# Kernel optimization log

Hardware: AMD Instinct MI355X
Metric: run time of the kernel (lower is better)

## Reference

```python
import jax, jax.numpy as jnp
import numpy as np

B, C, HIMG, WIMG = 32, 3, 224, 224
P, D, L, F, H, NC = 16, 768, 12, 3072, 12, 1000
S = (HIMG // P) * (WIMG // P)  # 196 tokens
DH = D // H                    # 64 per head


def setup_inputs() -> dict:
    key = jax.random.key(0)
    ks = jax.random.split(key, 12)
    rn = lambda i, shape, sc: jax.random.normal(ks[i], shape, jnp.float32) * sc
    return dict(
        x=rn(0, (B, C, HIMG, WIMG), 1.0),
        conv_w=rn(1, (D, C, P, P), 0.02),
        conv_b=jnp.zeros((D,), jnp.float32),
        pos_embed=rn(2, (S, D), 0.02),
        ln1_s=jnp.ones((L, D), jnp.float32),
        ln1_b=jnp.zeros((L, D), jnp.float32),
        wq=rn(3, (L, D, D), 0.02),
        wk=rn(4, (L, D, D), 0.02),
        wv=rn(5, (L, D, D), 0.02),
        ln2_s=jnp.ones((L, D), jnp.float32),
        ln2_b=jnp.zeros((L, D), jnp.float32),
        w1=rn(6, (L, D, F), 0.02),
        b1=jnp.zeros((L, F), jnp.float32),
        w2=rn(7, (L, F, D), 0.02),
        b2=jnp.zeros((L, D), jnp.float32),
        fc_w=rn(8, (D, NC), 0.02),
        fc_b=jnp.zeros((NC,), jnp.float32),
    )


def _layernorm(x, scale, bias, eps=1e-5):
    m = x.mean(-1, keepdims=True)
    v = ((x - m) ** 2).mean(-1, keepdims=True)
    return (x - m) * jax.lax.rsqrt(v + eps) * scale + bias


def reference(x, conv_w, conv_b, pos_embed, ln1_s, ln1_b, wq, wk, wv,
              ln2_s, ln2_b, w1, b1, w2, b2, fc_w, fc_b):
    # patch embedding: stride-P conv, then b c h w -> b (h w) c, add pos embed
    h = jax.lax.conv_general_dilated(
        x, conv_w, (P, P), 'VALID',
        dimension_numbers=('NCHW', 'OIHW', 'NCHW'))
    h = h + conv_b[None, :, None, None]
    h = h.reshape(B, D, S).transpose(0, 2, 1) + pos_embed  # [B,S,D]

    # NOTE: original scales attention logits by 1/sqrt(seq_len), not 1/sqrt(d_head)
    scale = 1.0 / jnp.sqrt(jnp.float32(S))

    def layer(hx, p):
        l1s, l1b, Wq, Wk, Wv, l2s, l2b, W1, B1, W2, B2 = p
        xn = _layernorm(hx, l1s, l1b)
        q = (xn @ Wq).reshape(B, S, H, DH)
        k = (xn @ Wk).reshape(B, S, H, DH)
        v = (xn @ Wv).reshape(B, S, H, DH)
        att = jax.nn.softmax(jnp.einsum('bshd,bthd->bhst', q, k) * scale, axis=-1)
        o = jnp.einsum('bhst,bthd->bshd', att, v).reshape(B, S, D)
        hx = hx + o
        y = _layernorm(hx, l2s, l2b) @ W1 + B1
        y = jax.nn.gelu(y, approximate=False) @ W2 + B2
        return hx + y, None

    h, _ = jax.lax.scan(layer, h, (ln1_s, ln1_b, wq, wk, wv,
                                   ln2_s, ln2_b, w1, b1, w2, b2))
    return h.mean(axis=1) @ fc_w + fc_b  # [B, num_classes]
```

## Files before the change

kernel.cpp:

```cpp
#include <hip/hip_runtime.h>
#include <hip/hip_bf16.h>

typedef __attribute__((ext_vector_type(8))) short bf16x8;
typedef __attribute__((ext_vector_type(4))) short bf16x4;
typedef __attribute__((ext_vector_type(4))) float f32x4;

#define DEVI static __device__ __forceinline__

DEVI unsigned short f2bf(float f) {
  __hip_bfloat16 h = __float2bfloat16(f);
  return __builtin_bit_cast(unsigned short, h);
}

DEVI f32x4 mfma16(bf16x8 a, bf16x8 b, f32x4 c) {
  return __builtin_amdgcn_mfma_f32_16x16x32_bf16(a, b, c, 0, 0, 0);
}

DEVI void gload16(const unsigned short* g, unsigned short* l) {
  __builtin_amdgcn_global_load_lds(
      (const __attribute__((address_space(1))) void*)g,
      (__attribute__((address_space(3))) void*)l, 16, 0, 0);
}

DEVI float erf_fast(float x) {
  float ax = fabsf(x);
  float t = 1.f / (1.f + 0.3275911f * ax);
  float poly = ((((1.061405429f * t - 1.453152027f) * t + 1.421413741f) * t -
                 0.284496736f) * t + 0.254829592f) * t;
  float e = __expf(-x * x);
  float er = 1.f - poly * e;
  return copysignf(er, x);
}

__global__ __launch_bounds__(256) void k_im2col(const float* __restrict__ x,
                                                unsigned short* __restrict__ A) {
  int t = blockIdx.x * 256 + threadIdx.x;
  int m = t / 192;
  int qq = t - m * 192;
  int kk = qq * 4;
  int c = kk >> 8;
  int r = kk & 255;
  int i = r >> 4;
  int j = r & 15;
  int b = m / 196;
  int s = m - b * 196;
  int ph = s / 14;
  int pw = s - ph * 14;
  const float* src = x + ((size_t)((b * 3 + c) * 224 + ph * 16 + i)) * 224 + pw * 16 + j;
  f32x4 v = *reinterpret_cast<const f32x4*>(src);
  bf16x4 o;
  o[0] = (short)f2bf(v[0]); o[1] = (short)f2bf(v[1]);
  o[2] = (short)f2bf(v[2]); o[3] = (short)f2bf(v[3]);
  *reinterpret_cast<bf16x4*>(A + (size_t)m * 768 + kk) = o;
}

__global__ __launch_bounds__(256) void k_cvt(const float* __restrict__ in,
                                             unsigned short* __restrict__ out) {
  int t = blockIdx.x * 256 + threadIdx.x;
  f32x4 v = *reinterpret_cast<const f32x4*>(in + (size_t)t * 4);
  bf16x4 o;
  o[0] = (short)f2bf(v[0]); o[1] = (short)f2bf(v[1]);
  o[2] = (short)f2bf(v[2]); o[3] = (short)f2bf(v[3]);
  *reinterpret_cast<bf16x4*>(out + (size_t)t * 4) = o;
}

DEVI void transpose_tile(const float* __restrict__ in, unsigned short* __restrict__ out,
                         int K, int N, int kt, int nt, unsigned short (*tile)[68]) {
  int r = threadIdx.x >> 4;
  int c4 = (threadIdx.x & 15) * 4;
  int k0 = kt * 64, n0 = nt * 64;
#pragma unroll
  for (int rr0 = 0; rr0 < 4; rr0++) {
    int rr = r + rr0 * 16;
    f32x4 v = *reinterpret_cast<const f32x4*>(in + (size_t)(k0 + rr) * N + n0 + c4);
    bf16x4 o;
    o[0] = (short)f2bf(v[0]); o[1] = (short)f2bf(v[1]);
    o[2] = (short)f2bf(v[2]); o[3] = (short)f2bf(v[3]);
    *reinterpret_cast<bf16x4*>(&tile[rr][c4]) = o;
  }
  __syncthreads();
#pragma unroll
  for (int rr0 = 0; rr0 < 4; rr0++) {
    int rr = r + rr0 * 16;
    bf16x4 o;
    o[0] = (short)tile[c4 + 0][rr];
    o[1] = (short)tile[c4 + 1][rr];
    o[2] = (short)tile[c4 + 2][rr];
    o[3] = (short)tile[c4 + 3][rr];
    *reinterpret_cast<bf16x4*>(out + (size_t)(n0 + rr) * K + k0 + c4) = o;
  }
}

__global__ __launch_bounds__(256) void k_wconvert(
    const float* __restrict__ wq, const float* __restrict__ wk, const float* __restrict__ wv,
    const float* __restrict__ w1, const float* __restrict__ w2,
    unsigned short* __restrict__ wqkvT, unsigned short* __restrict__ w1T,
    unsigned short* __restrict__ w2T) {
  __shared__ unsigned short tile[64][68];
  int bid = blockIdx.x;
  if (bid < 432) {
    int mm = bid / 144, t2 = bid - mm * 144;
    const float* in = (mm == 0) ? wq : ((mm == 1) ? wk : wv);
    transpose_tile(in, wqkvT + (size_t)mm * 768 * 768, 768, 768, t2 / 12, t2 % 12, tile);
  } else if (bid < 1008) {
    int t2 = bid - 432;
    transpose_tile(w1, w1T, 768, 3072, t2 / 48, t2 % 48, tile);
  } else {
    int t2 = bid - 1008;
    transpose_tile(w2, w2T, 3072, 768, t2 / 12, t2 % 12, tile);
  }
}

template <int RED>
__global__ __launch_bounds__(256) void k_ln(float* __restrict__ h,
                                            const float* __restrict__ part,
                                            const float* __restrict__ sc,
                                            const float* __restrict__ bi,
                                            unsigned short* __restrict__ xn) {
  int wave = threadIdx.x >> 6, lane = threadIdx.x & 63;
  int row = blockIdx.x * 4 + wave;
  float* hr = h + (size_t)row * 768;
  const float* pr = part + (size_t)row * 768;
  f32x4 v[3];
  float sum = 0.f;
#pragma unroll
  for (int i = 0; i < 3; i++) {
    v[i] = *reinterpret_cast<const f32x4*>(hr + i * 256 + lane * 4);
    if (RED) {
      f32x4 pv = *reinterpret_cast<const f32x4*>(pr + i * 256 + lane * 4);
#pragma unroll
      for (int c = 0; c < 4; c++) v[i][c] += pv[c];
      *reinterpret_cast<f32x4*>(hr + i * 256 + lane * 4) = v[i];
    }
    sum += v[i][0] + v[i][1] + v[i][2] + v[i][3];
  }
#pragma unroll
  for (int m = 1; m < 64; m <<= 1) sum += __shfl_xor(sum, m, 64);
  float mean = sum * (1.f / 768.f);
  float var = 0.f;
#pragma unroll
  for (int i = 0; i < 3; i++)
#pragma unroll
    for (int c = 0; c < 4; c++) { float d = v[i][c] - mean; var += d * d; }
#pragma unroll
  for (int m = 1; m < 64; m <<= 1) var += __shfl_xor(var, m, 64);
  float rs = rsqrtf(var * (1.f / 768.f) + 1e-5f);
#pragma unroll
  for (int i = 0; i < 3; i++) {
    int col = i * 256 + lane * 4;
    f32x4 s4 = *reinterpret_cast<const f32x4*>(sc + col);
    f32x4 b4 = *reinterpret_cast<const f32x4*>(bi + col);
    bf16x4 o;
#pragma unroll
    for (int c = 0; c < 4; c++) o[c] = (short)f2bf((v[i][c] - mean) * rs * s4[c] + b4[c]);
    *reinterpret_cast<bf16x4*>(xn + (size_t)row * 768 + col) = o;
  }
}

template <int EPI>
__global__ __launch_bounds__(256) void k_gemm(
    const unsigned short* __restrict__ A, const unsigned short* __restrict__ Bt, int K,
    int nks, const float* __restrict__ bias, const float* __restrict__ aux,
    float* __restrict__ outF, float* __restrict__ pOut) {
  __shared__ __align__(16) unsigned short As[2][128 * 32];
  __shared__ __align__(16) unsigned short Bs[2][128 * 32];

  int GX = gridDim.x, GY = gridDim.y, GZ = gridDim.z;
  int nb = GX * GY * GZ;
  int lin = (blockIdx.z * GY + blockIdx.y) * GX + blockIdx.x;
  int q = nb >> 3, r8 = nb & 7;
  int xcd = lin & 7, off = lin >> 3;
  int wid = (xcd < r8 ? xcd * (q + 1) : r8 * (q + 1) + (xcd - r8) * q) + off;
  int t2 = GX * GY;
  int sz = wid / t2;
  int w2 = wid - sz * t2;
  const int GM = 8;
  int per = GM * GX;
  int g = w2 / per;
  int first_m = g * GM;
  int gm = min(GM, GY - first_m);
  int rem = w2 - g * per;
  int mt = first_m + rem % gm;
  int nt = rem / gm;
  int m0 = mt * 128, n0 = nt * 128;
  int kb = sz * nks * 32;

  int tid = threadIdx.x;
  int wave = tid >> 6, lane = tid & 63;
  int wm = (wave >> 1) * 64, wn = (wave & 1) * 64;
  int lr = lane & 15, lg = lane >> 4;

  f32x4 acc[4][4];
  const f32x4 fz = {0.f, 0.f, 0.f, 0.f};
#pragma unroll
  for (int i = 0; i < 4; i++)
#pragma unroll
    for (int j = 0; j < 4; j++) acc[i][j] = fz;

  int srow = wave * 16 + (lane >> 2);
  int scol = (lane & 3) * 8;
  const unsigned short* Ag = A + (size_t)(m0 + srow) * K + scol + kb;
  const unsigned short* Bg = Bt + (size_t)(n0 + srow) * K + scol + kb;
  int lofs = wave * 16 * 32;

#pragma unroll
  for (int j = 0; j < 2; j++) {
    gload16(Ag + (size_t)j * 64 * K, &As[0][lofs + j * 64 * 32]);
    gload16(Bg + (size_t)j * 64 * K, &Bs[0][lofs + j * 64 * 32]);
  }
  __syncthreads();

  for (int kt = 0; kt < nks - 1; kt++) {
    int cur = kt & 1;
    int k0 = (kt + 1) << 5;
#pragma unroll
    for (int j = 0; j < 2; j++) {
      gload16(Ag + (size_t)j * 64 * K + k0, &As[cur ^ 1][lofs + j * 64 * 32]);
      gload16(Bg + (size_t)j * 64 * K + k0, &Bs[cur ^ 1][lofs + j * 64 * 32]);
    }
    bf16x8 a[4], b[4];
#pragma unroll
    for (int i = 0; i < 4; i++) {
      a[i] = *reinterpret_cast<const bf16x8*>(&As[cur][(wm + i * 16 + lr) * 32 + lg * 8]);
      b[i] = *reinterpret_cast<const bf16x8*>(&Bs[cur][(wn + i * 16 + lr) * 32 + lg * 8]);
    }
#pragma unroll
    for (int mi = 0; mi < 4; mi++)
#pragma unroll
      for (int ni = 0; ni < 4; ni++) acc[mi][ni] = mfma16(a[mi], b[ni], acc[mi][ni]);
    __syncthreads();
  }
  {
    int cur = (nks - 1) & 1;
    bf16x8 a[4], b[4];
#pragma unroll
    for (int i = 0; i < 4; i++) {
      a[i] = *reinterpret_cast<const bf16x8*>(&As[cur][(wm + i * 16 + lr) * 32 + lg * 8]);
      b[i] = *reinterpret_cast<const bf16x8*>(&Bs[cur][(wn + i * 16 + lr) * 32 + lg * 8]);
    }
#pragma unroll
    for (int mi = 0; mi < 4; mi++)
#pragma unroll
      for (int ni = 0; ni < 4; ni++) acc[mi][ni] = mfma16(a[mi], b[ni], acc[mi][ni]);
  }

#pragma unroll
  for (int mi = 0; mi < 4; mi++) {
    int mb = m0 + wm + mi * 16 + lg * 4;
    int bb = mb / 196;
    int s0 = mb - bb * 196;
#pragma unroll
    for (int ni = 0; ni < 4; ni++) {
      int n = n0 + wn + ni * 16 + lr;
      int s = s0;
#pragma unroll
      for (int r = 0; r < 4; r++) {
        int m = mb + r;
        float val = acc[mi][ni][r];
        if (EPI == 0) {
          outF[(size_t)m * 768 + n] = val + bias[n] + aux[(size_t)s * 768 + n];
          s++;
          if (s == 196) s = 0;
        } else {
          if (sz == 0) outF[(size_t)m * 768 + n] += val + bias[n];
          else pOut[(size_t)m * 768 + n] = val;
        }
      }
    }
  }
}

__global__ __launch_bounds__(256) void k_mean_r(const float* __restrict__ h,
                                                const float* __restrict__ part,
                                                float* __restrict__ hm) {
  int b = blockIdx.x, d = blockIdx.y * 256 + threadIdx.x;
  float acc = 0.f;
  for (int s = 0; s < 196; s++) {
    size_t i = (size_t)(b * 196 + s) * 768 + d;
    acc += h[i] + part[i];
  }
  hm[b * 768 + d] = acc * (1.f / 196.f);
}

template <int EPI>
__global__ __launch_bounds__(512, 2) void k_gemm256p(
    const unsigned short* __restrict__ A, const unsigned short* __restrict__ Bt,
    const float* __restrict__ bias, unsigned short* __restrict__ outB) {
  const int K = 768, NK = 24;
  __shared__ __align__(16) unsigned short LDS[4][16384];
  const int MVALID = 6272;

  int GX = gridDim.x, GY = gridDim.y;
  int nb = GX * GY;
  int lin = blockIdx.y * GX + blockIdx.x;
  int q = nb >> 3, r8 = nb & 7;
  int xcd = lin & 7, off = lin >> 3;
  int wid = (xcd < r8 ? xcd * (q + 1) : r8 * (q + 1) + (xcd - r8) * q) + off;
  const int GM = 4;
  int per = GM * GX;
  int g = wid / per;
  int first_m = g * GM;
  int gm = min(GM, GY - first_m);
  int rem = wid - g * per;
  int mt = first_m + rem % gm;
  int nt = rem / gm;
  int m0 = mt * 256, n0 = nt * 256;

  int tid = threadIdx.x;
  int w = tid >> 6, lane = tid & 63;
  int wm = w >> 2, wn = w & 3;
  int lr = lane & 15, lg = lane >> 4;

  f32x4 acc[8][4];
  const f32x4 fz = {0.f, 0.f, 0.f, 0.f};
#pragma unroll
  for (int i = 0; i < 8; i++)
#pragma unroll
    for (int j = 0; j < 4; j++) acc[i][j] = fz;

  int srow = w * 16 + (lane >> 2);
  int scol = ((lane & 3) ^ ((lane >> 3) & 3)) * 8;
  const unsigned short* Ag = A + (size_t)(m0 + srow) * K + scol;
  const unsigned short* Bg = Bt + (size_t)(n0 + srow) * K + scol;
  int ldst = w * 512;

  int colsw = (lg ^ ((lr >> 1) & 3)) * 8;
  int rofA = wm * 4096 + lr * 32 + colsw;
  int rofB = 8192 + wn * 2048 + lr * 32 + colsw;

#define STAGEA(kt)                                                          \
  {                                                                         \
    unsigned short* d_ = &LDS[(kt) & 3][0];                                 \
    const unsigned short* a_ = Ag + (kt) * 32;                              \
    gload16(a_, d_ + ldst);                                                 \
    gload16(a_ + (size_t)128 * K, d_ + 4096 + ldst);                        \
  }
#define STAGEB(kt)                                                          \
  {                                                                         \
    unsigned short* d_ = &LDS[(kt) & 3][0];                                 \
    const unsigned short* b_ = Bg + (kt) * 32;                              \
    gload16(b_, d_ + 8192 + ldst);                                          \
    gload16(b_ + (size_t)128 * K, d_ + 12288 + ldst);                       \
  }

#define KTILE(ktv, VMSTR, STG, LAST)                                         \
  {                                                                          \
    const int kt_ = (ktv);                                                   \
    const unsigned short* buf_ = &LDS[kt_ & 3][0];                           \
    bf16x8 afr[8], bfr[2];                                                   \
    _Pragma("unroll") for (int mi = 0; mi < 8; mi++) afr[mi] =               \
        *reinterpret_cast<const bf16x8*>(buf_ + rofA + mi * 512);            \
    _Pragma("unroll") for (int ni = 0; ni < 2; ni++) bfr[ni] =               \
        *reinterpret_cast<const bf16x8*>(buf_ + rofB + ni * 512);            \
    if (STG) STAGEA(kt_ + 3);                                                \
    asm volatile("s_waitcnt lgkmcnt(0)" ::: "memory");                       \
    __builtin_amdgcn_sched_barrier(0);                                       \
    __builtin_amdgcn_s_setprio(1);                                           \
    _Pragma("unroll") for (int mi = 0; mi < 8; mi++)                         \
        _Pragma("unroll") for (int ni = 0; ni < 2; ni++)                     \
            acc[mi][ni] = mfma16(afr[mi], bfr[ni], acc[mi][ni]);             \
    __builtin_amdgcn_s_setprio(0);                                           \
    __builtin_amdgcn_s_barrier();                                            \
    _Pragma("unroll") for (int ni = 0; ni < 2; ni++) bfr[ni] =               \
        *reinterpret_cast<const bf16x8*>(buf_ + rofB + (2 + ni) * 512);      \
    if (STG) STAGEB(kt_ + 3);                                                \
    asm volatile("s_waitcnt lgkmcnt(0)" ::: "memory");                       \
    __builtin_amdgcn_sched_barrier(0);                                       \
    __builtin_amdgcn_s_setprio(1);                                           \
    _Pragma("unroll") for (int mi = 0; mi < 8; mi++)                         \
        _Pragma("unroll") for (int ni = 0; ni < 2; ni++)                     \
            acc[mi][2 + ni] = mfma16(afr[mi], bfr[ni], acc[mi][2 + ni]);     \
    __builtin_amdgcn_s_setprio(0);                                           \
    if (!LAST) {                                                             \
      asm volatile("s_waitcnt vmcnt(" VMSTR ")" ::: "memory");               \
      __builtin_amdgcn_s_barrier();                                          \
    }                                                                        \
  }

  STAGEA(0); STAGEB(0);
  STAGEA(1); STAGEB(1);
  STAGEA(2); STAGEB(2);
  asm volatile("s_waitcnt vmcnt(8)" ::: "memory");
  __builtin_amdgcn_s_barrier();

  for (int kt = 0; kt < NK - 3; kt++) KTILE(kt, "8", true, false);
  KTILE(NK - 3, "4", false, false);
  KTILE(NK - 2, "0", false, false);
  KTILE(NK - 1, "0", false, true);
#undef KTILE
#undef STAGEA
#undef STAGEB

  if (EPI == 1) {
#pragma unroll
    for (int ni = 0; ni < 4; ni++) {
      int n = n0 + wn * 64 + ni * 16 + lr;
      int which = (n >= 1536) ? 2 : ((n >= 768) ? 1 : 0);
      int n7 = n - which * 768;
      int hd = n7 >> 6, dh = n7 & 63;
      unsigned short* ob = outB + (size_t)which * 4816896 + dh;
#pragma unroll
      for (int mi = 0; mi < 8; mi++) {
        int mb = m0 + wm * 128 + mi * 16 + lg * 4;
        if (mb >= MVALID) continue;
        int bb = mb / 196;
        int s = mb - bb * 196;
#pragma unroll
        for (int r = 0; r < 4; r++) {
          ob[((size_t)((bb * 12 + hd) * 196 + s) << 6)] = f2bf(acc[mi][ni][r]);
          s++;
          if (s == 196) { s = 0; bb++; }
        }
      }
    }
  } else {
#pragma unroll
    for (int mi = 0; mi < 8; mi++) {
      int mb = m0 + wm * 128 + mi * 16 + lg * 4;
      if (mb >= MVALID) continue;
#pragma unroll
      for (int ni = 0; ni < 4; ni++) {
        int n = n0 + wn * 64 + ni * 16 + lr;
#pragma unroll
        for (int r = 0; r < 4; r++) {
          int m = mb + r;
          float u = acc[mi][ni][r] + bias[n];
          float gg = 0.5f * u * (1.f + erf_fast(u * 0.70710678118654752f));
          outB[(size_t)m * 3072 + n] = f2bf(gg);
        }
      }
    }
  }
}

__global__ __launch_bounds__(512) void k_attn(const unsigned short* __restrict__ q,
                                              const unsigned short* __restrict__ k,
                                              const unsigned short* __restrict__ v,
                                              float* __restrict__ h) {
  __shared__ __align__(16) unsigned short Kl[208][72];
  __shared__ __align__(16) unsigned short Vt[64][248];
  __shared__ __align__(16) unsigned short Sc[8][16][232];
  int bh = blockIdx.x;
  int b = bh / 12, hh = bh - b * 12;
  size_t base = (size_t)bh * 196 * 64;
  int tid = threadIdx.x, wave = tid >> 6, lane = tid & 63;
  int lr = lane & 15, lg = lane >> 4;

  const bf16x8 bz = {0, 0, 0, 0, 0, 0, 0, 0};
  for (int u = tid; u < 208 * 8; u += 512) {
    int row = u >> 3, c8 = (u & 7) * 8;
    bf16x8 val = bz;
    if (row < 196) val = *reinterpret_cast<const bf16x8*>(k + base + row * 64 + c8);
    *reinterpret_cast<bf16x8*>(&Kl[row][c8]) = val;
  }
  for (int u = tid; u < 224 * 8; u += 512) {
    int t = u >> 3, d8 = (u & 7) * 8;
    bf16x8 val = bz;
    if (t < 196) val = *reinterpret_cast<const bf16x8*>(v + base + t * 64 + d8);
#pragma unroll
    for (int i = 0; i < 8; i++) Vt[d8 + i][t] = (unsigned short)val[i];
  }
  for (int i2 = lane; i2 < 256; i2 += 64) Sc[wave][i2 >> 4][208 + (i2 & 15)] = 0;
  __syncthreads();

  const float scale = 1.f / 14.f;
  for (int st = wave; st < 13; st += 8) {
    int qb = st * 16;
    int s = qb + lr;
    bf16x8 aq0 = bz, aq1 = bz;
    if (s < 196) {
      aq0 = *reinterpret_cast<const bf16x8*>(q + base + (size_t)s * 64 + lg * 8);
      aq1 = *reinterpret_cast<const bf16x8*>(q + base + (size_t)s * 64 + 32 + lg * 8);
    }
    f32x4 sc[13];
#pragma unroll
    for (int t = 0; t < 13; t++) {
      bf16x8 bk0 = *reinterpret_cast<const bf16x8*>(&Kl[t * 16 + lr][lg * 8]);
      bf16x8 bk1 = *reinterpret_cast<const bf16x8*>(&Kl[t * 16 + lr][32 + lg * 8]);
      f32x4 z = {0.f, 0.f, 0.f, 0.f};
      z = mfma16(aq0, bk0, z);
      z = mfma16(aq1, bk1, z);
      sc[t] = z;
    }
    float mx[4] = {-1e30f, -1e30f, -1e30f, -1e30f};
#pragma unroll
    for (int t = 0; t < 13; t++) {
      int tc = t * 16 + lr;
#pragma unroll
      for (int r = 0; r < 4; r++) {
        float xv = (tc < 196) ? sc[t][r] * scale : -1e30f;
        sc[t][r] = xv;
        mx[r] = fmaxf(mx[r], xv);
      }
    }
#pragma unroll
    for (int r = 0; r < 4; r++)
#pragma unroll
      for (int mm = 1; mm < 16; mm <<= 1) mx[r] = fmaxf(mx[r], __shfl_xor(mx[r], mm, 64));
    float sm[4] = {0.f, 0.f, 0.f, 0.f};
#pragma unroll
    for (int t = 0; t < 13; t++)
#pragma unroll
      for (int r = 0; r < 4; r++) {
        float e = __expf(sc[t][r] - mx[r]);
        sc[t][r] = e;
        sm[r] += e;
      }
#pragma unroll
    for (int r = 0; r < 4; r++)
#pragma unroll
      for (int mm = 1; mm < 16; mm <<= 1) sm[r] += __shfl_xor(sm[r], mm, 64);
    float inv[4];
#pragma unroll
    for (int r = 0; r < 4; r++) inv[r] = 1.f / sm[r];
#pragma unroll
    for (int t = 0; t < 13; t++)
#pragma unroll
      for (int r = 0; r < 4; r++)
        Sc[wave][lg * 4 + r][t * 16 + lr] = f2bf(sc[t][r] * inv[r]);
    asm volatile("s_waitcnt lgkmcnt(0)" ::: "memory");
    bf16x8 ap[7];
#pragma unroll
    for (int ks = 0; ks < 7; ks++)
      ap[ks] = *reinterpret_cast<const bf16x8*>(&Sc[wave][lr][ks * 32 + lg * 8]);
#pragma unroll
    for (int nt = 0; nt < 4; nt++) {
      f32x4 o = {0.f, 0.f, 0.f, 0.f};
#pragma unroll
      for (int ks = 0; ks < 7; ks++) {
        bf16x8 bv = *reinterpret_cast<const bf16x8*>(&Vt[nt * 16 + lr][ks * 32 + lg * 8]);
        o = mfma16(ap[ks], bv, o);
      }
#pragma unroll
      for (int r = 0; r < 4; r++) {
        int s2 = qb + lg * 4 + r;
        if (s2 < 196) h[(size_t)(b * 196 + s2) * 768 + hh * 64 + nt * 16 + lr] += o[r];
      }
    }
  }
}

__global__ __launch_bounds__(256) void k_fc(const float* __restrict__ hm,
                                            const float* __restrict__ w,
                                            const float* __restrict__ bias,
                                            float* __restrict__ out) {
  int b = blockIdx.x, n = blockIdx.y * 256 + threadIdx.x;
  if (n >= 1000) return;
  float acc = bias[n];
  for (int d = 0; d < 768; d++) acc += hm[b * 768 + d] * w[d * 1000 + n];
  out[b * 1000 + n] = acc;
}

extern "C" void kernel_launch(void* const* d_in, const int* in_sizes, int n_in,
                              void* d_out, int out_size, void* d_ws, size_t ws_size,
                              hipStream_t stream) {
  const float* x      = (const float*)d_in[0];
  const float* conv_w = (const float*)d_in[1];
  const float* conv_b = (const float*)d_in[2];
  const float* pos    = (const float*)d_in[3];
  const float* ln1_s  = (const float*)d_in[4];
  const float* ln1_b  = (const float*)d_in[5];
  const float* wq     = (const float*)d_in[6];
  const float* wk     = (const float*)d_in[7];
  const float* wv     = (const float*)d_in[8];
  const float* ln2_s  = (const float*)d_in[9];
  const float* ln2_b  = (const float*)d_in[10];
  const float* w1     = (const float*)d_in[11];
  const float* b1     = (const float*)d_in[12];
  const float* w2     = (const float*)d_in[13];
  const float* b2     = (const float*)d_in[14];
  const float* fc_w   = (const float*)d_in[15];
  const float* fc_b   = (const float*)d_in[16];
  float* out = (float*)d_out;

  char* p = (char*)d_ws;
  auto alloc = [&](size_t bytes) {
    char* r = p;
    p += (bytes + 255) & ~(size_t)255;
    return r;
  };
  const size_t M = 6272, MP = 6400, QSZ = 4816896;
  float* h              = (float*)alloc(M * 768 * 4);
  unsigned short* xn    = (unsigned short*)alloc(MP * 768 * 2);
  unsigned short* qkv   = (unsigned short*)alloc(3 * QSZ * 2);
  unsigned short* y1    = (unsigned short*)alloc(MP * 3072 * 2);
  unsigned short* wqkvT = (unsigned short*)alloc((size_t)2304 * 768 * 2);
  unsigned short* w1T   = (unsigned short*)alloc((size_t)3072 * 768 * 2);
  unsigned short* w2T   = (unsigned short*)alloc((size_t)3072 * 768 * 2);
  float* hm             = (float*)alloc(32 * 768 * 4);
  unsigned short* cwB   = qkv;
  float* part           = (float*)qkv;

  k_cvt<<<576, 256, 0, stream>>>(conv_w, cwB);
  k_im2col<<<4704, 256, 0, stream>>>(x, xn);
  k_gemm<0><<<dim3(6, 49, 1), 256, 0, stream>>>(xn, cwB, 768, 24, conv_b, pos, h, nullptr);

  for (int l = 0; l < 12; l++) {
    k_wconvert<<<1584, 256, 0, stream>>>(
        wq + (size_t)l * 589824, wk + (size_t)l * 589824, wv + (size_t)l * 589824,
        w1 + (size_t)l * 2359296, w2 + (size_t)l * 2359296, wqkvT, w1T, w2T);
    if (l == 0)
      k_ln<0><<<1568, 256, 0, stream>>>(h, nullptr, ln1_s, ln1_b, xn);
    else
      k_ln<1><<<1568, 256, 0, stream>>>(h, part, ln1_s + l * 768, ln1_b + l * 768, xn);
    k_gemm256p<1><<<dim3(9, 25), 512, 0, stream>>>(xn, wqkvT, nullptr, qkv);
    k_attn<<<384, 512, 0, stream>>>(qkv, qkv + QSZ, qkv + 2 * QSZ, h);
    k_ln<0><<<1568, 256, 0, stream>>>(h, nullptr, ln2_s + l * 768, ln2_b + l * 768, xn);
    k_gemm256p<2><<<dim3(12, 25), 512, 0, stream>>>(xn, w1T, b1 + (size_t)l * 3072, y1);
    k_gemm<3><<<dim3(6, 49, 2), 256, 0, stream>>>(y1, w2T, 3072, 48, b2 + (size_t)l * 768,
                                                  nullptr, h, part);
  }
  k_mean_r<<<dim3(32, 3), 256, 0, stream>>>(h, part, hm);
  k_fc<<<dim3(32, 4), 256, 0, stream>>>(hm, fc_w, fc_b, out);
}
```

Before: 2.923 ms.

## Hoist all-layer weight conversion into one launch and narrow W2 GEMM tile

When workspace allows, all 12 layers' weights are transposed and converted to bf16 in a single large kernel before the layer loop, replacing 12 per-layer conversion launches that sat on the critical path between layers. The k_gemm kernel is templated on the N tile width, and the FFN down-projection now uses 128x64 tiles with twice as many blocks to improve occupancy and load balance. This costs more workspace memory and reduces per-block reuse in the W2 GEMM.

```diff
diff --git a/kernel.cpp b/kernel.cpp
--- a/kernel.cpp
+++ b/kernel.cpp
@@ -91,13 +91,11 @@
   }
 }
 
-__global__ __launch_bounds__(256) void k_wconvert(
-    const float* __restrict__ wq, const float* __restrict__ wk, const float* __restrict__ wv,
-    const float* __restrict__ w1, const float* __restrict__ w2,
-    unsigned short* __restrict__ wqkvT, unsigned short* __restrict__ w1T,
-    unsigned short* __restrict__ w2T) {
-  __shared__ unsigned short tile[64][68];
-  int bid = blockIdx.x;
+DEVI void wconvert_body(const float* wq, const float* wk, const float* wv,
+                        const float* w1, const float* w2,
+                        unsigned short* wqkvT, unsigned short* w1T,
+                        unsigned short* w2T, int bid,
+                        unsigned short (*tile)[68]) {
   if (bid < 432) {
     int mm = bid / 144, t2 = bid - mm * 144;
     const float* in = (mm == 0) ? wq : ((mm == 1) ? wk : wv);
@@ -109,6 +107,28 @@
     int t2 = bid - 1008;
     transpose_tile(w2, w2T, 3072, 768, t2 / 12, t2 % 12, tile);
   }
+}
+
+__global__ __launch_bounds__(256) void k_wconvert(
+    const float* __restrict__ wq, const float* __restrict__ wk, const float* __restrict__ wv,
+    const float* __restrict__ w1, const float* __restrict__ w2,
+    unsigned short* __restrict__ wqkvT, unsigned short* __restrict__ w1T,
+    unsigned short* __restrict__ w2T) {
+  __shared__ unsigned short tile[64][68];
+  wconvert_body(wq, wk, wv, w1, w2, wqkvT, w1T, w2T, blockIdx.x, tile);
+}
+
+__global__ __launch_bounds__(256) void k_wconvert_all(
+    const float* __restrict__ wq, const float* __restrict__ wk, const float* __restrict__ wv,
+    const float* __restrict__ w1, const float* __restrict__ w2,
+    unsigned short* __restrict__ wqkvT, unsigned short* __restrict__ w1T,
+    unsigned short* __restrict__ w2T) {
+  __shared__ unsigned short tile[64][68];
+  int l = blockIdx.x / 1584, bid = blockIdx.x - l * 1584;
+  wconvert_body(wq + (size_t)l * 589824, wk + (size_t)l * 589824, wv + (size_t)l * 589824,
+                w1 + (size_t)l * 2359296, w2 + (size_t)l * 2359296,
+                wqkvT + (size_t)l * 1769472, w1T + (size_t)l * 2359296,
+                w2T + (size_t)l * 2359296, bid, tile);
 }
 
 template <int RED>
@@ -157,13 +177,15 @@
   }
 }
 
-template <int EPI>
+template <int EPI, int BN>
 __global__ __launch_bounds__(256) void k_gemm(
     const unsigned short* __restrict__ A, const unsigned short* __restrict__ Bt, int K,
     int nks, const float* __restrict__ bias, const float* __restrict__ aux,
     float* __restrict__ outF, float* __restrict__ pOut) {
+  constexpr int NI = BN / 32;
+  constexpr int BR = BN / 64;
   __shared__ __align__(16) unsigned short As[2][128 * 32];
-  __shared__ __align__(16) unsigned short Bs[2][128 * 32];
+  __shared__ __align__(16) unsigned short Bs[2][BN * 32];
 
   int GX = gridDim.x, GY = gridDim.y, GZ = gridDim.z;
   int nb = GX * GY * GZ;
@@ -182,20 +204,20 @@
   int rem = w2 - g * per;
   int mt = first_m + rem % gm;
   int nt = rem / gm;
-  int m0 = mt * 128, n0 = nt * 128;
+  int m0 = mt * 128, n0 = nt * BN;
   int kb = sz * nks * 32;
 
   int tid = threadIdx.x;
   int wave = tid >> 6, lane = tid & 63;
-  int wm = (wave >> 1) * 64, wn = (wave & 1) * 64;
+  int wm = (wave >> 1) * 64, wn = (wave & 1) * (NI * 16);
   int lr = lane & 15, lg = lane >> 4;
 
-  f32x4 acc[4][4];
+  f32x4 acc[4][NI];
   const f32x4 fz = {0.f, 0.f, 0.f, 0.f};
 #pragma unroll
   for (int i = 0; i < 4; i++)
 #pragma unroll
-    for (int j = 0; j < 4; j++) acc[i][j] = fz;
+    for (int j = 0; j < NI; j++) acc[i][j] = fz;
 
   int srow = wave * 16 + (lane >> 2);
   int scol = (lane & 3) * 8;
@@ -204,44 +226,48 @@
   int lofs = wave * 16 * 32;
 
 #pragma unroll
-  for (int j = 0; j < 2; j++) {
+  for (int j = 0; j < 2; j++)
     gload16(Ag + (size_t)j * 64 * K, &As[0][lofs + j * 64 * 32]);
+#pragma unroll
+  for (int j = 0; j < BR; j++)
     gload16(Bg + (size_t)j * 64 * K, &Bs[0][lofs + j * 64 * 32]);
-  }
   __syncthreads();
 
   for (int kt = 0; kt < nks - 1; kt++) {
     int cur = kt & 1;
     int k0 = (kt + 1) << 5;
 #pragma unroll
-    for (int j = 0; j < 2; j++) {
+    for (int j = 0; j < 2; j++)
       gload16(Ag + (size_t)j * 64 * K + k0, &As[cur ^ 1][lofs + j * 64 * 32]);
+#pragma unroll
+    for (int j = 0; j < BR; j++)
       gload16(Bg + (size_t)j * 64 * K + k0, &Bs[cur ^ 1][lofs + j * 64 * 32]);
-    }
-    bf16x8 a[4], b[4];
-#pragma unroll
-    for (int i = 0; i < 4; i++) {
+    bf16x8 a[4], b[NI];
+#pragma unroll
+    for (int i = 0; i < 4; i++)
       a[i] = *reinterpret_cast<const bf16x8*>(&As[cur][(wm + i * 16 + lr) * 32 + lg * 8]);
+#pragma unroll
+    for (int i = 0; i < NI; i++)
       b[i] = *reinterpret_cast<const bf16x8*>(&Bs[cur][(wn + i * 16 + lr) * 32 + lg * 8]);
-    }
 #pragma unroll
     for (int mi = 0; mi < 4; mi++)
 #pragma unroll
-      for (int ni = 0; ni < 4; ni++) acc[mi][ni] = mfma16(a[mi], b[ni], acc[mi][ni]);
+      for (int ni = 0; ni < NI; ni++) acc[mi][ni] = mfma16(a[mi], b[ni], acc[mi][ni]);
     __syncthreads();
   }
   {
     int cur = (nks - 1) & 1;
-    bf16x8 a[4], b[4];
-#pragma unroll
-    for (int i = 0; i < 4; i++) {
+    bf16x8 a[4], b[NI];
+#pragma unroll
+    for (int i = 0; i < 4; i++)
       a[i] = *reinterpret_cast<const bf16x8*>(&As[cur][(wm + i * 16 + lr) * 32 + lg * 8]);
+#pragma unroll
+    for (int i = 0; i < NI; i++)
       b[i] = *reinterpret_cast<const bf16x8*>(&Bs[cur][(wn + i * 16 + lr) * 32 + lg * 8]);
-    }
 #pragma unroll
     for (int mi = 0; mi < 4; mi++)
 #pragma unroll
-      for (int ni = 0; ni < 4; ni++) acc[mi][ni] = mfma16(a[mi], b[ni], acc[mi][ni]);
+      for (int ni = 0; ni < NI; ni++) acc[mi][ni] = mfma16(a[mi], b[ni], acc[mi][ni]);
   }
 
 #pragma unroll
@@ -250,7 +276,7 @@
     int bb = mb / 196;
     int s0 = mb - bb * 196;
 #pragma unroll
-    for (int ni = 0; ni < 4; ni++) {
+    for (int ni = 0; ni < NI; ni++) {
       int n = n0 + wn + ni * 16 + lr;
       int s = s0;
 #pragma unroll
@@ -584,31 +610,45 @@
   unsigned short* xn    = (unsigned short*)alloc(MP * 768 * 2);
   unsigned short* qkv   = (unsigned short*)alloc(3 * QSZ * 2);
   unsigned short* y1    = (unsigned short*)alloc(MP * 3072 * 2);
-  unsigned short* wqkvT = (unsigned short*)alloc((size_t)2304 * 768 * 2);
-  unsigned short* w1T   = (unsigned short*)alloc((size_t)3072 * 768 * 2);
-  unsigned short* w2T   = (unsigned short*)alloc((size_t)3072 * 768 * 2);
   float* hm             = (float*)alloc(32 * 768 * 4);
+
+  size_t used = (size_t)(p - (char*)d_ws);
+  size_t perL = ((size_t)2304 * 768 + 2 * (size_t)3072 * 768) * 2;
+  bool hoist = ws_size >= used + 12 * perL + 4096;
+  int nw = hoist ? 12 : 1;
+  unsigned short* wqkvT = (unsigned short*)alloc((size_t)nw * 2304 * 768 * 2);
+  unsigned short* w1T   = (unsigned short*)alloc((size_t)nw * 3072 * 768 * 2);
+  unsigned short* w2T   = (unsigned short*)alloc((size_t)nw * 3072 * 768 * 2);
+
   unsigned short* cwB   = qkv;
   float* part           = (float*)qkv;
 
   k_cvt<<<576, 256, 0, stream>>>(conv_w, cwB);
   k_im2col<<<4704, 256, 0, stream>>>(x, xn);
-  k_gemm<0><<<dim3(6, 49, 1), 256, 0, stream>>>(xn, cwB, 768, 24, conv_b, pos, h, nullptr);
+  k_gemm<0, 128><<<dim3(6, 49, 1), 256, 0, stream>>>(xn, cwB, 768, 24, conv_b, pos, h,
+                                                     nullptr);
+  if (hoist)
+    k_wconvert_all<<<19008, 256, 0, stream>>>(wq, wk, wv, w1, w2, wqkvT, w1T, w2T);
 
   for (int l = 0; l < 12; l++) {
-    k_wconvert<<<1584, 256, 0, stream>>>(
-        wq + (size_t)l * 589824, wk + (size_t)l * 589824, wv + (size_t)l * 589824,
-        w1 + (size_t)l * 2359296, w2 + (size_t)l * 2359296, wqkvT, w1T, w2T);
+    unsigned short* wqkvT_l = wqkvT + (hoist ? (size_t)l * 1769472 : 0);
+    unsigned short* w1T_l   = w1T + (hoist ? (size_t)l * 2359296 : 0);
+    unsigned short* w2T_l   = w2T + (hoist ? (size_t)l * 2359296 : 0);
+    if (!hoist)
+      k_wconvert<<<1584, 256, 0, stream>>>(
+          wq + (size_t)l * 589824, wk + (size_t)l * 589824, wv + (size_t)l * 589824,
+          w1 + (size_t)l * 2359296, w2 + (size_t)l * 2359296, wqkvT_l, w1T_l, w2T_l);
     if (l == 0)
       k_ln<0><<<1568, 256, 0, stream>>>(h, nullptr, ln1_s, ln1_b, xn);
     else
       k_ln<1><<<1568, 256, 0, stream>>>(h, part, ln1_s + l * 768, ln1_b + l * 768, xn);
-    k_gemm256p<1><<<dim3(9, 25), 512, 0, stream>>>(xn, wqkvT, nullptr, qkv);
+    k_gemm256p<1><<<dim3(9, 25), 512, 0, stream>>>(xn, wqkvT_l, nullptr, qkv);
     k_attn<<<384, 512, 0, stream>>>(qkv, qkv + QSZ, qkv + 2 * QSZ, h);
     k_ln<0><<<1568, 256, 0, stream>>>(h, nullptr, ln2_s + l * 768, ln2_b + l * 768, xn);
-    k_gemm256p<2><<<dim3(12, 25), 512, 0, stream>>>(xn, w1T, b1 + (size_t)l * 3072, y1);
-    k_gemm<3><<<dim3(6, 49, 2), 256, 0, stream>>>(y1, w2T, 3072, 48, b2 + (size_t)l * 768,
-                                                  nullptr, h, part);
+    k_gemm256p<2><<<dim3(12, 25), 512, 0, stream>>>(xn, w1T_l, b1 + (size_t)l * 3072, y1);
+    k_gemm<3, 64><<<dim3(12, 49, 2), 256, 0, stream>>>(y1, w2T_l, 3072, 48,
+                                                       b2 + (size_t)l * 768, nullptr, h,
+                                                       part);
   }
   k_mean_r<<<dim3(32, 3), 256, 0, stream>>>(h, part, hm);
   k_fc<<<dim3(32, 4), 256, 0, stream>>>(hm, fc_w, fc_b, out);
```

Measured after the change: 2.847 ms. 2.6% less time.
